# Kernel tuning notes

Hardware: AMD Instinct MI355X
Metric: run time of the kernel (lower is better)

Reference implementation:

```python
import jax, jax.numpy as jnp
import numpy as np
from jax import lax

TAU = 1.0
SIGMAS = (1.0, 1.0, 1.0)
SIGMA_CUTOFF = 2.0
SCALE_FACTORS = (0.5, 1.0)
ITERATIONS = (4, 4)
EPS = 1e-6


def _grid(shape):
    # identity sampling grid in voxel coordinates, (3, D, H, W)
    return jnp.stack(jnp.meshgrid(*[jnp.arange(s, dtype=jnp.float32) for s in shape], indexing='ij'), axis=0)


def warp(vol, flow):
    # vol (B,C,D,H,W), flow (B,3,D,H,W) voxel-space displacements; trilinear, zeros padding
    g = _grid(vol.shape[2:])
    def one_b(v, f):
        coords = g + f  # (3,D,H,W)
        def one_c(ch):
            return jax.scipy.ndimage.map_coordinates(ch, [coords[0], coords[1], coords[2]], order=1, mode='constant', cval=0.0)
        return jax.vmap(one_c)(v)
    return jax.vmap(one_b)(vol, flow)


def gaussian_smooth(x, sigmas=SIGMAS):
    # separable depthwise Gaussian, kernel radius = ceil(sigma_cutoff * sigma)
    C = x.shape[1]
    for axis, sigma in enumerate(sigmas):
        r = int(np.ceil(SIGMA_CUTOFF * sigma))
        t = jnp.arange(-r, r + 1, dtype=x.dtype)
        k = jnp.exp(-0.5 * (t / sigma) ** 2)
        k = k / k.sum()
        kshape = [1, 1, 1, 1, 1]
        kshape[2 + axis] = k.size
        w = jnp.broadcast_to(k.reshape(kshape), (C, 1) + tuple(kshape[2:]))
        x = lax.conv_general_dilated(x, w, (1, 1, 1), 'SAME', feature_group_count=C,
                                     dimension_numbers=('NCDHW', 'OIDHW', 'NCDHW'))
    return x


def _gradient(x, axis):
    # np.gradient style: central diff interior, one-sided at edges, unit spacing
    lo = lax.slice_in_dim(x, 1, 2, axis=axis) - lax.slice_in_dim(x, 0, 1, axis=axis)
    mid = (lax.slice_in_dim(x, 2, None, axis=axis) - lax.slice_in_dim(x, 0, -2, axis=axis)) * 0.5
    hi = lax.slice_in_dim(x, -1, None, axis=axis) - lax.slice_in_dim(x, -2, -1, axis=axis)
    return jnp.concatenate([lo, mid, hi], axis=axis)


def demon_forces(moving, fixed):
    # active demons: gradient of (warped) moving image, (B,1,D,H,W) -> (B,3,D,H,W)
    m = moving[:, 0]
    grads = jnp.stack([_gradient(m, 1), _gradient(m, 2), _gradient(m, 3)], axis=1)
    diff = moving - fixed  # (B,1,D,H,W)
    denom = jnp.sum(grads ** 2, axis=1, keepdims=True) + diff ** 2
    return grads * diff / (denom + EPS)


def resize_tri(x, shape):
    return jax.image.resize(x, x.shape[:2] + tuple(shape), method='trilinear')


def match_vf(vf, shape):
    if tuple(vf.shape[2:]) == tuple(shape):
        return vf
    old = vf.shape[2:]
    out = resize_tri(vf, shape)
    scale = jnp.array([s1 / s2 for s1, s2 in zip(shape, old)], dtype=vf.dtype).reshape(1, 3, 1, 1, 1)
    return out * scale


def run_level(vf, img_s, mask_s, cond_s, iters):
    def body(i, carry):
        vf, _ = carry
        warped = warp(cond_s, vf)
        f = demon_forces(warped, img_s)
        vf = vf - TAU * (f * mask_s)
        vf = gaussian_smooth(vf)
        return (vf, warped)
    return lax.fori_loop(0, iters, body, (vf, jnp.zeros_like(cond_s)))


def conv3d(x, w, b=None):
    y = lax.conv_general_dilated(x, w, (1, 1, 1), 'SAME', dimension_numbers=('NCDHW', 'OIDHW', 'NCDHW'))
    return y if b is None else y + b[None, :, None, None, None]


def instance_norm(x, eps=1e-5):
    m = x.mean(axis=(2, 3, 4), keepdims=True)
    v = x.var(axis=(2, 3, 4), keepdims=True)
    return (x - m) * lax.rsqrt(v + eps)


def mish(x):
    return x * jnp.tanh(jax.nn.softplus(x))


def setup_inputs() -> dict:
    key = jax.random.key(0)
    ks = jax.random.split(key, 8)
    S = (1, 1, 96, 96, 96)
    image = jax.random.normal(ks[0], S, dtype=jnp.float32)
    conditional = jax.random.normal(ks[1], S, dtype=jnp.float32)
    mask = jnp.ones(S, dtype=jnp.float32)
    w1 = jax.random.normal(ks[2], (32, 5, 3, 3, 3), dtype=jnp.float32) * 0.05
    w2 = jax.random.normal(ks[3], (64, 32, 3, 3, 3), dtype=jnp.float32) * 0.05
    w3 = jax.random.normal(ks[4], (32, 64, 3, 3, 3), dtype=jnp.float32) * 0.05
    w4 = jax.random.normal(ks[5], (3, 32, 3, 3, 3), dtype=jnp.float32) * 0.05
    b4 = jnp.zeros((3,), dtype=jnp.float32)
    return {"image": image, "mask": mask, "conditional": conditional,
            "w1": w1, "w2": w2, "w3": w3, "w4": w4, "b4": b4}


def reference(image, mask, conditional, w1, w2, w3, w4, b4):
    full_shape = image.shape[2:]
    vf = None
    warped = None
    for sf, iters in zip(SCALE_FACTORS, ITERATIONS):
        shp = tuple(int(s * sf) for s in full_shape)
        img_s = resize_tri(image, shp)
        mask_s = jax.image.resize(mask, mask.shape[:2] + shp, method='nearest')
        cond_s = resize_tri(conditional, shp)
        if vf is None:
            vf = jnp.zeros((image.shape[0], 3) + shp, image.dtype)
        else:
            vf = match_vf(vf, shp)
        vf, warped = run_level(vf, img_s, mask_s, cond_s, iters)
    # correction network on full-resolution level outputs
    masked_image = image * mask
    stacked = jnp.concatenate([vf, masked_image, warped], axis=1)  # (B,5,D,H,W)
    h = mish(instance_norm(conv3d(stacked, w1)))
    h = mish(instance_norm(conv3d(h, w2)))
    h = mish(instance_norm(conv3d(h, w3)))
    corr = conv3d(h, w4, b4)
    cvf = gaussian_smooth(vf + corr)
    vf_full = match_vf(vf, full_shape)
    cvf_full = match_vf(cvf, full_shape)
    corrected_warped = warp(conditional, cvf_full)
    warped_full = warp(conditional, vf_full)
    return (corrected_warped, warped_full, cvf_full, vf_full)
```

## Files before the change

kernel.cpp:

```cpp
#include <hip/hip_runtime.h>
#include <math.h>

typedef unsigned short ushort_t;
typedef __attribute__((ext_vector_type(8))) short bf16x8;
typedef __attribute__((ext_vector_type(4))) float f32x4;

constexpr int V96 = 96 * 96 * 96;
constexpr int V48 = 48 * 48 * 48;
constexpr int V98 = 98 * 98 * 98;

__device__ __constant__ float GK[5] = {
    0.05448868454964294f, 0.24420134240717082f, 0.40261994608637245f,
    0.24420134240717082f, 0.05448868454964294f };

__device__ __forceinline__ float bf2f(ushort_t u) {
    return __uint_as_float(((unsigned)u) << 16);
}
__device__ __forceinline__ ushort_t f2bf(float f) {
    unsigned x = __float_as_uint(f);
    x += 0x7fffu + ((x >> 16) & 1u);
    return (ushort_t)(x >> 16);
}
__device__ __forceinline__ bool is_bf16(const unsigned* mrw) {
    return mrw[0] == 0x3F803F80u;
}
__device__ __forceinline__ float ld_in(const void* p, int i, bool bf) {
    return bf ? bf2f(((const ushort_t*)p)[i]) : ((const float*)p)[i];
}

constexpr size_t OFF_IMG32 = 0;
constexpr size_t OFF_MSK32 = OFF_IMG32 + V96;
constexpr size_t OFF_COND32 = OFF_MSK32 + V96;
constexpr size_t OFF_VF96 = OFF_COND32 + V96;
constexpr size_t OFF_WTS = OFF_VF96 + 3 * (size_t)V96;
constexpr size_t OFF_ST = OFF_WTS + 117760;
constexpr size_t OFF_PK1 = OFF_ST + 256;
constexpr size_t OFF_PK2 = OFF_PK1 + 3584;
constexpr size_t OFF_PK3 = OFF_PK2 + 27648;
constexpr size_t OFF_PK4 = OFF_PK3 + 27648;
constexpr size_t OFF_B = OFF_PK4 + 6912;
constexpr size_t BSZF = 32 * (size_t)V98 / 2;
constexpr size_t OFF_C = OFF_B + BSZF;
constexpr size_t CSZF = 64 * (size_t)V98;
constexpr size_t WS_FLOATS = OFF_C + CSZF / 2;

constexpr size_t WOB = 117504;

template<int S>
__device__ __forceinline__ void decomp(int r, int& z, int& y, int& x) {
    z = r / (S * S); int r2 = r - z * S * S; y = r2 / S; x = r2 - y * S;
}

__global__ void cvt_in_k(const void* __restrict__ in, float* __restrict__ out, int n,
                         const unsigned* __restrict__ mrw) {
    int i = blockIdx.x * 256 + threadIdx.x;
    if (i >= n) return;
    out[i] = ld_in(in, i, is_bf16(mrw));
}
__global__ void cvt3_k(const void* __restrict__ a, const void* __restrict__ b,
                       const void* __restrict__ c, float* __restrict__ oa,
                       float* __restrict__ ob, float* __restrict__ oc,
                       const unsigned* __restrict__ mrw) {
    int i = blockIdx.x * 256 + threadIdx.x;
    if (i >= V96) return;
    bool bf = is_bf16(mrw);
    oa[i] = ld_in(a, i, bf);
    ob[i] = ld_in(b, i, bf);
    oc[i] = ld_in(c, i, bf);
}
__global__ void store_out_k(const float* __restrict__ in, void* __restrict__ out,
                            size_t off, int n, const unsigned* __restrict__ mrw) {
    int i = blockIdx.x * 256 + threadIdx.x;
    if (i >= n) return;
    if (is_bf16(mrw)) ((ushort_t*)out)[off + i] = f2bf(in[i]);
    else              ((float*)out)[off + i] = in[i];
}

template<int C>
__global__ void zero_pad_k(ushort_t* __restrict__ buf) {
    int v = blockIdx.x * 256 + threadIdx.x;
    if (v >= V98) return;
    int z = v / (98 * 98); int r = v - z * 98 * 98; int y = r / 98; int x = r - y * 98;
    if (z != 0 && z != 97 && y != 0 && y != 97 && x != 0 && x != 97) return;
    bf16x8 zv = {};
    bf16x8* p = (bf16x8*)(buf + (size_t)v * C);
#pragma unroll
    for (int c = 0; c < C / 8; ++c) p[c] = zv;
}

__global__ void pack1_k(const void* __restrict__ w, ushort_t* __restrict__ pk,
                        const unsigned* __restrict__ mrw) {
    int i = blockIdx.x * 256 + threadIdx.x;
    if (i >= 7168) return;
    bool bf = is_bf16(mrw);
    int j = i & 7, n = (i >> 3) & 15, ng = (i >> 7) & 1, tq = i >> 8;
    int co = ng * 16 + n;
    float v = (tq < 27 && j < 5) ? ld_in(w, (co * 5 + j) * 27 + tq, bf) : 0.f;
    pk[i] = f2bf(v);
}
__global__ void pack2_k(const void* __restrict__ w, ushort_t* __restrict__ pk,
                        const unsigned* __restrict__ mrw) {
    int i = blockIdx.x * 256 + threadIdx.x;
    if (i >= 55296) return;
    bool bf = is_bf16(mrw);
    int j = i & 7, n = (i >> 3) & 15, q = (i >> 7) & 3, ng = (i >> 9) & 3, t = i >> 11;
    int co = ng * 16 + n, ci = q * 8 + j;
    pk[i] = f2bf(ld_in(w, (co * 32 + ci) * 27 + t, bf));
}
__global__ void pack3_k(const void* __restrict__ w, ushort_t* __restrict__ pk,
                        const unsigned* __restrict__ mrw) {
    int i = blockIdx.x * 256 + threadIdx.x;
    if (i >= 55296) return;
    bool bf = is_bf16(mrw);
    int j = i & 7, n = (i >> 3) & 15, q = (i >> 7) & 3, ng = (i >> 9) & 1, kb = (i >> 10) & 1, t = i >> 11;
    int co = ng * 16 + n, ci = kb * 32 + q * 8 + j;
    pk[i] = f2bf(ld_in(w, (co * 64 + ci) * 27 + t, bf));
}
__global__ void pack4_k(const void* __restrict__ w, ushort_t* __restrict__ pk,
                        const unsigned* __restrict__ mrw) {
    int i = blockIdx.x * 256 + threadIdx.x;
    if (i >= 13824) return;
    bool bf = is_bf16(mrw);
    int j = i & 7, m = (i >> 3) & 15, q = (i >> 7) & 3, t = i >> 9;
    int ci = q * 8 + j;
    float v = (m < 3) ? ld_in(w, (m * 32 + ci) * 27 + t, bf) : 0.f;
    pk[i] = f2bf(v);
}

__device__ __forceinline__ int ds_wt(int i, float w[4]) {
    int j0 = 2 * i - 1;
    w[0] = 0.25f; w[1] = 0.75f; w[2] = 0.75f; w[3] = 0.25f;
    float s = 0.f;
#pragma unroll
    for (int t = 0; t < 4; ++t) { int j = j0 + t; if (j < 0 || j > 95) w[t] = 0.f; s += w[t]; }
    float inv = 1.f / s;
#pragma unroll
    for (int t = 0; t < 4; ++t) w[t] *= inv;
    return j0;
}

__global__ void down_tri_k(const float* __restrict__ in, float* __restrict__ out) {
    int idx = blockIdx.x * 256 + threadIdx.x;
    if (idx >= V48) return;
    int z, y, x; decomp<48>(idx, z, y, x);
    float wz[4], wy[4], wx[4];
    int z0 = ds_wt(z, wz), y0 = ds_wt(y, wy), x0 = ds_wt(x, wx);
    float acc = 0.f;
#pragma unroll
    for (int a = 0; a < 4; ++a) {
        int zz = z0 + a; zz = zz < 0 ? 0 : (zz > 95 ? 95 : zz);
#pragma unroll
        for (int b = 0; b < 4; ++b) {
            int yy = y0 + b; yy = yy < 0 ? 0 : (yy > 95 ? 95 : yy);
            float wzy = wz[a] * wy[b];
#pragma unroll
            for (int c = 0; c < 4; ++c) {
                int xx = x0 + c; xx = xx < 0 ? 0 : (xx > 95 ? 95 : xx);
                acc = fmaf(wzy * wx[c], in[(zz * 96 + yy) * 96 + xx], acc);
            }
        }
    }
    out[idx] = acc;
}

__global__ void down_near_k(const float* __restrict__ in, float* __restrict__ out) {
    int idx = blockIdx.x * 256 + threadIdx.x;
    if (idx >= V48) return;
    int z, y, x; decomp<48>(idx, z, y, x);
    out[idx] = in[((2 * z + 1) * 96 + (2 * y + 1)) * 96 + (2 * x + 1)];
}

__device__ __forceinline__ void up_c(int i, int& i0, float& t) {
    float s = 0.5f * (float)i - 0.25f;
    s = fminf(fmaxf(s, 0.f), 47.f);
    int ii = (int)s; if (ii > 46) ii = 46;
    i0 = ii; t = s - (float)ii;
}

__global__ void up_vf_k(const float* __restrict__ in, float* __restrict__ out) {
    int idx = blockIdx.x * 256 + threadIdx.x;
    if (idx >= 3 * V96) return;
    int c = idx / V96; int r = idx - c * V96;
    int z, y, x; decomp<96>(r, z, y, x);
    int z0, y0, x0; float tz, ty, tx;
    up_c(z, z0, tz); up_c(y, y0, ty); up_c(x, x0, tx);
    const float* p = in + (size_t)c * V48;
    float acc = 0.f;
#pragma unroll
    for (int a = 0; a < 2; ++a)
#pragma unroll
        for (int b = 0; b < 2; ++b)
#pragma unroll
            for (int d = 0; d < 2; ++d) {
                float w = (a ? tz : 1.f - tz) * (b ? ty : 1.f - ty) * (d ? tx : 1.f - tx);
                acc = fmaf(w, p[((z0 + a) * 48 + (y0 + b)) * 48 + (x0 + d)], acc);
            }
    out[idx] = 2.f * acc;
}

template<int S>
__global__ void warp_k(const float* __restrict__ vol, const float* __restrict__ flow,
                       float* __restrict__ out) {
    constexpr int S3 = S * S * S;
    int idx = blockIdx.x * 256 + threadIdx.x;
    if (idx >= S3) return;
    int z, y, x; decomp<S>(idx, z, y, x);
    float cz = (float)z + flow[idx];
    float cy = (float)y + flow[S3 + idx];
    float cx = (float)x + flow[2 * S3 + idx];
    float fz = floorf(cz), fy = floorf(cy), fx = floorf(cx);
    int iz = (int)fz, iy = (int)fy, ix = (int)fx;
    float tz = cz - fz, ty = cy - fy, tx = cx - fx;
    float acc = 0.f;
#pragma unroll
    for (int a = 0; a < 2; ++a)
#pragma unroll
        for (int b = 0; b < 2; ++b)
#pragma unroll
            for (int c = 0; c < 2; ++c) {
                int zz = iz + a, yy = iy + b, xx = ix + c;
                float w = (a ? tz : 1.f - tz) * (b ? ty : 1.f - ty) * (c ? tx : 1.f - tx);
                bool ok = ((unsigned)zz < (unsigned)S) && ((unsigned)yy < (unsigned)S) &&
                          ((unsigned)xx < (unsigned)S);
                float v = ok ? vol[(zz * S + yy) * S + xx] : 0.f;
                acc = fmaf(w, v, acc);
            }
    out[idx] = acc;
}

__global__ void warp_out_k(const float* __restrict__ vol, const float* __restrict__ flow,
                           void* __restrict__ out, size_t off,
                           const unsigned* __restrict__ mrw) {
    constexpr int S = 96, S3 = V96;
    int idx = blockIdx.x * 256 + threadIdx.x;
    if (idx >= S3) return;
    int z, y, x; decomp<S>(idx, z, y, x);
    float cz = (float)z + flow[idx];
    float cy = (float)y + flow[S3 + idx];
    float cx = (float)x + flow[2 * S3 + idx];
    float fz = floorf(cz), fy = floorf(cy), fx = floorf(cx);
    int iz = (int)fz, iy = (int)fy, ix = (int)fx;
    float tz = cz - fz, ty = cy - fy, tx = cx - fx;
    float acc = 0.f;
#pragma unroll
    for (int a = 0; a < 2; ++a)
#pragma unroll
        for (int b = 0; b < 2; ++b)
#pragma unroll
            for (int c = 0; c < 2; ++c) {
                int zz = iz + a, yy = iy + b, xx = ix + c;
                float w = (a ? tz : 1.f - tz) * (b ? ty : 1.f - ty) * (c ? tx : 1.f - tx);
                bool ok = ((unsigned)zz < (unsigned)S) && ((unsigned)yy < (unsigned)S) &&
                          ((unsigned)xx < (unsigned)S);
                float v = ok ? vol[(zz * S + yy) * S + xx] : 0.f;
                acc = fmaf(w, v, acc);
            }
    if (is_bf16(mrw)) ((ushort_t*)out)[off + idx] = f2bf(acc);
    else              ((float*)out)[off + idx] = acc;
}

template<int S>
__global__ void demon4_k(const float* __restrict__ wv, const float* __restrict__ fx_,
                         const float* __restrict__ msk, const float* __restrict__ vin,
                         float* __restrict__ vout) {
    constexpr int S3 = S * S * S;
    int u = blockIdx.x * 256 + threadIdx.x;
    if (u >= S3 / 4) return;
    int idx = u * 4;
    int z, y, x0; decomp<S>(idx, z, y, x0);
    float w[12];
    *(float4*)(w + 4) = *(const float4*)(wv + idx);
    if (x0 > 0) *(float4*)(w + 0) = *(const float4*)(wv + idx - 4);
    else { w[0] = w[1] = w[2] = w[3] = 0.f; }
    if (x0 < S - 4) *(float4*)(w + 8) = *(const float4*)(wv + idx + 4);
    else { w[8] = w[9] = w[10] = w[11] = 0.f; }
    float zp[4], zm[4], yp[4], ym[4];
    float sz = (z == 0 || z == S - 1) ? 1.f : 0.5f;
    float sy = (y == 0 || y == S - 1) ? 1.f : 0.5f;
    if (z > 0) *(float4*)zm = *(const float4*)(wv + idx - S * S);
    else { zm[0] = w[4]; zm[1] = w[5]; zm[2] = w[6]; zm[3] = w[7]; }
    if (z < S - 1) *(float4*)zp = *(const float4*)(wv + idx + S * S);
    else { zp[0] = w[4]; zp[1] = w[5]; zp[2] = w[6]; zp[3] = w[7]; }
    if (y > 0) *(float4*)ym = *(const float4*)(wv + idx - S);
    else { ym[0] = w[4]; ym[1] = w[5]; ym[2] = w[6]; ym[3] = w[7]; }
    if (y < S - 1) *(float4*)yp = *(const float4*)(wv + idx + S);
    else { yp[0] = w[4]; yp[1] = w[5]; yp[2] = w[6]; yp[3] = w[7]; }
    float fx4[4], mk4[4], v0[4], v1[4], v2[4], o0[4], o1[4], o2[4];
    *(float4*)fx4 = *(const float4*)(fx_ + idx);
    *(float4*)mk4 = *(const float4*)(msk + idx);
    *(float4*)v0 = *(const float4*)(vin + idx);
    *(float4*)v1 = *(const float4*)(vin + S3 + idx);
    *(float4*)v2 = *(const float4*)(vin + 2 * S3 + idx);
#pragma unroll
    for (int j = 0; j < 4; ++j) {
        int x = x0 + j;
        float m = w[4 + j];
        float gz = sz * (zp[j] - zm[j]);
        float gy = sy * (yp[j] - ym[j]);
        float gx = (x == 0) ? (w[j + 5] - w[j + 4])
                 : (x == S - 1) ? (w[j + 4] - w[j + 3])
                 : 0.5f * (w[j + 5] - w[j + 3]);
        float diff = m - fx4[j];
        float denom = gz * gz + gy * gy + gx * gx + diff * diff + 1e-6f;
        float r = diff / denom;
        float mk = mk4[j] * r;
        o0[j] = v0[j] - gz * mk;
        o1[j] = v1[j] - gy * mk;
        o2[j] = v2[j] - gx * mk;
    }
    *(float4*)(vout + idx) = *(float4*)o0;
    *(float4*)(vout + S3 + idx) = *(float4*)o1;
    *(float4*)(vout + 2 * S3 + idx) = *(float4*)o2;
}

template<int S, int ZC>
__global__ void smooth3d_k(const float* __restrict__ in, float* __restrict__ out) {
    constexpr int NZ = S / ZC;
    int idx = blockIdx.x * 256 + threadIdx.x;
    if (idx >= 3 * NZ * S * S) return;
    int x = idx % S;
    int y = (idx / S) % S;
    int zci = (idx / (S * S)) % NZ;
    int c = idx / (S * S * NZ);
    int z0 = zci * ZC;
    const float* p = in + (size_t)c * (S * S * S);
    float* o = out + (size_t)c * (S * S * S) + ((size_t)z0 * S + y) * S + x;
    float wx[5], wy[5];
    int xc[5], yc[5];
#pragma unroll
    for (int t = 0; t < 5; ++t) {
        int xx = x + t - 2, yy = y + t - 2;
        wx[t] = ((unsigned)xx < (unsigned)S) ? GK[t] : 0.f;
        xc[t] = xx < 0 ? 0 : (xx >= S ? S - 1 : xx);
        wy[t] = ((unsigned)yy < (unsigned)S) ? GK[t] : 0.f;
        yc[t] = yy < 0 ? 0 : (yy >= S ? S - 1 : yy);
    }
    float win[5] = {0.f, 0.f, 0.f, 0.f, 0.f};
#pragma unroll 1
    for (int k = 0; k < ZC + 4; ++k) {
        int zz = z0 - 2 + k;
        int zcl = zz < 0 ? 0 : (zz >= S ? S - 1 : zz);
        const float* ps = p + (size_t)zcl * S * S;
        float s = 0.f;
#pragma unroll
        for (int ty = 0; ty < 5; ++ty) {
            const float* pr = ps + yc[ty] * S;
            float rs = 0.f;
#pragma unroll
            for (int tx = 0; tx < 5; ++tx)
                rs = fmaf(wx[tx], pr[xc[tx]], rs);
            s = fmaf(wy[ty], rs, s);
        }
        s = ((unsigned)zz < (unsigned)S) ? s : 0.f;
        win[0] = win[1]; win[1] = win[2]; win[2] = win[3]; win[3] = win[4]; win[4] = s;
        if (k >= 4)
            o[(size_t)(k - 4) * S * S] =
                fmaf(GK[0], win[0], fmaf(GK[1], win[1], fmaf(GK[2], win[2],
                fmaf(GK[3], win[3], GK[4] * win[4]))));
    }
}

__global__ void build_st8_k(const float* __restrict__ vf, const float* __restrict__ img,
                            const float* __restrict__ msk, const float* __restrict__ wrp,
                            ushort_t* __restrict__ st8) {
    int idx = blockIdx.x * 256 + threadIdx.x;
    if (idx >= V96) return;
    int z, y, x; decomp<96>(idx, z, y, x);
    size_t pa = ((size_t)(z + 1) * 98 + (y + 1)) * 98 + (x + 1);
    union { bf16x8 v; ushort_t u[8]; } w;
    w.u[0] = f2bf(vf[idx]);
    w.u[1] = f2bf(vf[V96 + idx]);
    w.u[2] = f2bf(vf[2 * V96 + idx]);
    w.u[3] = f2bf(img[idx] * msk[idx]);
    w.u[4] = f2bf(wrp[idx]);
    w.u[5] = 0; w.u[6] = 0; w.u[7] = 0;
    *(bf16x8*)(st8 + pa * 8) = w.v;
}

__global__ __launch_bounds__(256) void conv1_mfma_k(const ushort_t* __restrict__ st8,
                                                    const ushort_t* __restrict__ pk,
                                                    ushort_t* __restrict__ out,
                                                    float* __restrict__ part) {
    const int tid = threadIdx.x;
    const int lane = tid & 63;
    const int wv = tid >> 6;
    const int ng = wv & 1;
    const int vs = wv >> 1;
    const int m = lane & 15;
    const int q = lane >> 4;
    const int x0 = blockIdx.x * 32 + vs * 16;
    const int y = blockIdx.y, z = blockIdx.z;
    f32x4 acc = {0.f, 0.f, 0.f, 0.f};
#pragma unroll
    for (int g = 0; g < 7; ++g) {
        int t = g * 4 + q;
        size_t pa = 0;
        if (t < 27) {
            int dz = t / 9, dy = (t / 3) % 3, dx = t % 3;
            pa = (((size_t)(z + dz) * 98) + (y + dy)) * 98 + (x0 + dx + m);
        }
        bf16x8 a = *(const bf16x8*)(st8 + pa * 8);
        bf16x8 b = *(const bf16x8*)(pk + (((size_t)t * 2 + ng) * 16 + m) * 8);
        acc = __builtin_amdgcn_mfma_f32_16x16x32_bf16(a, b, acc, 0, 0, 0);
    }
    const size_t pb = (((size_t)(z + 1) * 98) + (y + 1)) * 98 + (x0 + 1);
#pragma unroll
    for (int r = 0; r < 4; ++r) {
        int mm = q * 4 + r;
        out[(pb + mm) * 32 + ng * 16 + m] = f2bf(acc[r]);
    }
    float s = acc[0] + acc[1] + acc[2] + acc[3];
    float sq = acc[0] * acc[0] + acc[1] * acc[1] + acc[2] * acc[2] + acc[3] * acc[3];
    s += __shfl_xor(s, 16);  s += __shfl_xor(s, 32);
    sq += __shfl_xor(sq, 16); sq += __shfl_xor(sq, 32);
    __shared__ float red[4][2][16];
    if (q == 0) { red[wv][0][m] = s; red[wv][1][m] = sq; }
    __syncthreads();
    if (tid < 64) {
        int which = tid >> 5;
        int c = tid & 31;
        int cg = c >> 4, cm = c & 15;
        float v = red[cg][which][cm] + red[cg + 2][which][cm];
        size_t row = ((size_t)blockIdx.z * 96 + blockIdx.y) * 3 + blockIdx.x;
        part[row * 64 + tid] = v;
    }
}

__global__ __launch_bounds__(256, 3) void conv2_lds_k(const ushort_t* __restrict__ in,
                                                      const ushort_t* __restrict__ pk,
                                                      ushort_t* __restrict__ out,
                                                      float* __restrict__ part) {
    __shared__ bf16x8 sm[2160];
    const int tid = threadIdx.x;
    const int X0 = blockIdx.x * 16, Y0 = blockIdx.y * 4, Z0 = blockIdx.z * 2;
    for (int cid = tid; cid < 1728; cid += 256) {
        int r = cid / 72, c = cid - r * 72;
        int zz = r / 6, yy = r - zz * 6;
        int v = c >> 2, sub = c & 3;
        const bf16x8* gp = (const bf16x8*)(in +
            (((size_t)(Z0 + zz) * 98 + (Y0 + yy)) * 98 + X0 + v) * 32) + sub;
        sm[r * 90 + v * 5 + sub] = *gp;
    }
    __syncthreads();
    const int lane = tid & 63;
    const int wv = tid >> 6;
    const int w2 = wv >> 1;
    const int nh = wv & 1;
    const int m = lane & 15;
    const int q = lane >> 4;
    f32x4 acc[2][2][2] = {};
#pragma unroll 1
    for (int dx = 0; dx < 3; ++dx) {
        bf16x8 a[16];
#pragma unroll
        for (int zp = 0; zp < 4; ++zp)
#pragma unroll
            for (int iy = 0; iy < 4; ++iy)
                a[zp * 4 + iy] = sm[(zp * 6 + w2 * 2 + iy) * 90 + (dx + m) * 5 + q];
#pragma unroll
        for (int dz = 0; dz < 3; ++dz)
#pragma unroll
            for (int dy = 0; dy < 3; ++dy) {
                const int t = (dz * 3 + dy) * 3 + dx;
#pragma unroll
                for (int ngl = 0; ngl < 2; ++ngl) {
                    const int ng = nh * 2 + ngl;
                    bf16x8 b = *(const bf16x8*)(pk + ((((size_t)t * 4 + ng) * 4 + q) * 16 + m) * 8);
#pragma unroll
                    for (int z = 0; z < 2; ++z)
#pragma unroll
                        for (int yy = 0; yy < 2; ++yy)
                            acc[z][yy][ngl] = __builtin_amdgcn_mfma_f32_16x16x32_bf16(
                                a[(z + dz) * 4 + (yy + dy)], b, acc[z][yy][ngl], 0, 0, 0);
                }
            }
    }
#pragma unroll
    for (int z = 0; z < 2; ++z)
#pragma unroll
        for (int yy = 0; yy < 2; ++yy) {
            const size_t pb = (((size_t)(Z0 + z + 1) * 98) + (Y0 + w2 * 2 + yy + 1)) * 98 + (X0 + 1);
#pragma unroll
            for (int ngl = 0; ngl < 2; ++ngl) {
                const int ng = nh * 2 + ngl;
#pragma unroll
                for (int r = 0; r < 4; ++r) {
                    int mm = q * 4 + r;
                    out[(pb + mm) * 64 + ng * 16 + m] = f2bf(acc[z][yy][ngl][r]);
                }
            }
        }
    float s0 = 0.f, q0 = 0.f, s1 = 0.f, q1 = 0.f;
#pragma unroll
    for (int z = 0; z < 2; ++z)
#pragma unroll
        for (int yy = 0; yy < 2; ++yy)
#pragma unroll
            for (int r = 0; r < 4; ++r) {
                float v0 = acc[z][yy][0][r]; s0 += v0; q0 = fmaf(v0, v0, q0);
                float v1 = acc[z][yy][1][r]; s1 += v1; q1 = fmaf(v1, v1, q1);
            }
    s0 += __shfl_xor(s0, 16); s0 += __shfl_xor(s0, 32);
    q0 += __shfl_xor(q0, 16); q0 += __shfl_xor(q0, 32);
    s1 += __shfl_xor(s1, 16); s1 += __shfl_xor(s1, 32);
    q1 += __shfl_xor(q1, 16); q1 += __shfl_xor(q1, 32);
    __shared__ float red[4][2][2][16];
    if (q == 0) {
        red[wv][0][0][m] = s0; red[wv][0][1][m] = q0;
        red[wv][1][0][m] = s1; red[wv][1][1][m] = q1;
    }
    __syncthreads();
    if (tid < 128) {
        int which = tid >> 6;
        int c = tid & 63;
        int cnh = (c >> 5) & 1, cngl = (c >> 4) & 1, cm = c & 15;
        float v = red[cnh][cngl][which][cm] + red[2 + cnh][cngl][which][cm];
        size_t row = ((size_t)blockIdx.z * 24 + blockIdx.y) * 6 + blockIdx.x;
        part[row * 128 + tid] = v;
    }
}

__global__ __launch_bounds__(256, 4) void conv3_lds_k(const ushort_t* __restrict__ in,
                                                      const ushort_t* __restrict__ pk,
                                                      ushort_t* __restrict__ out,
                                                      float* __restrict__ part) {
    __shared__ bf16x8 sm[2160];
    const int tid = threadIdx.x;
    const int X0 = blockIdx.x * 16, Y0 = blockIdx.y * 4, Z0 = blockIdx.z * 2;
    const int lane = tid & 63;
    const int wv = tid >> 6;
    const int w2 = wv >> 1;
    const int ng = wv & 1;
    const int m = lane & 15;
    const int q = lane >> 4;
    f32x4 acc[2][2] = {};
#pragma unroll 1
    for (int kb = 0; kb < 2; ++kb) {
        if (kb) __syncthreads();
        for (int cid = tid; cid < 1728; cid += 256) {
            int r = cid / 72, c = cid - r * 72;
            int zz = r / 6, yy = r - zz * 6;
            int v = c >> 2, sub = c & 3;
            const bf16x8* gp = (const bf16x8*)(in +
                (((size_t)(Z0 + zz) * 98 + (Y0 + yy)) * 98 + X0 + v) * 64 + kb * 32) + sub;
            sm[r * 90 + v * 5 + sub] = *gp;
        }
        __syncthreads();
#pragma unroll 1
        for (int dx = 0; dx < 3; ++dx) {
            bf16x8 a[16];
#pragma unroll
            for (int zp = 0; zp < 4; ++zp)
#pragma unroll
                for (int iy = 0; iy < 4; ++iy)
                    a[zp * 4 + iy] = sm[(zp * 6 + w2 * 2 + iy) * 90 + (dx + m) * 5 + q];
#pragma unroll
            for (int dz = 0; dz < 3; ++dz)
#pragma unroll
                for (int dy = 0; dy < 3; ++dy) {
                    const int t = (dz * 3 + dy) * 3 + dx;
                    bf16x8 b = *(const bf16x8*)(pk +
                        (((((size_t)t * 2 + kb) * 2 + ng) * 4 + q) * 16 + m) * 8);
#pragma unroll
                    for (int z = 0; z < 2; ++z)
#pragma unroll
                        for (int yy = 0; yy < 2; ++yy)
                            acc[z][yy] = __builtin_amdgcn_mfma_f32_16x16x32_bf16(
                                a[(z + dz) * 4 + (yy + dy)], b, acc[z][yy], 0, 0, 0);
                }
        }
    }
#pragma unroll
    for (int z = 0; z < 2; ++z)
#pragma unroll
        for (int yy = 0; yy < 2; ++yy) {
            const size_t pb = (((size_t)(Z0 + z + 1) * 98) + (Y0 + w2 * 2 + yy + 1)) * 98 + (X0 + 1);
#pragma unroll
            for (int r = 0; r < 4; ++r) {
                int mm = q * 4 + r;
                out[(pb + mm) * 32 + ng * 16 + m] = f2bf(acc[z][yy][r]);
            }
        }
    float s = 0.f, sq = 0.f;
#pragma unroll
    for (int z = 0; z < 2; ++z)
#pragma unroll
        for (int yy = 0; yy < 2; ++yy)
#pragma unroll
            for (int r = 0; r < 4; ++r) {
                float v = acc[z][yy][r]; s += v; sq = fmaf(v, v, sq);
            }
    s += __shfl_xor(s, 16);  s += __shfl_xor(s, 32);
    sq += __shfl_xor(sq, 16); sq += __shfl_xor(sq, 32);
    __shared__ float red[4][2][16];
    if (q == 0) { red[wv][0][m] = s; red[wv][1][m] = sq; }
    __syncthreads();
    if (tid < 64) {
        int which = tid >> 5;
        int c = tid & 31;
        int cg = c >> 4, cm = c & 15;
        float v = red[cg][which][cm] + red[cg + 2][which][cm];
        size_t row = ((size_t)blockIdx.z * 24 + blockIdx.y) * 6 + blockIdx.x;
        part[row * 64 + tid] = v;
    }
}

__global__ __launch_bounds__(384) void conv4_mfma_k(const ushort_t* __restrict__ in,
                                                    const ushort_t* __restrict__ pk,
                                                    const float* __restrict__ bias,
                                                    const float* __restrict__ vf,
                                                    float* __restrict__ out) {
    const int lane = threadIdx.x & 63;
    const int wv = threadIdx.x >> 6;
    const int n = lane & 15;
    const int q = lane >> 4;
    const int x0 = wv * 16;
    const int y = blockIdx.y, z = blockIdx.z;
    f32x4 acc = {0.f, 0.f, 0.f, 0.f};
#pragma unroll 1
    for (int dz = 0; dz < 3; ++dz)
#pragma unroll
        for (int dy = 0; dy < 3; ++dy)
#pragma unroll
            for (int dx = 0; dx < 3; ++dx) {
                const int t = (dz * 3 + dy) * 3 + dx;
                bf16x8 a = *(const bf16x8*)(pk + (((size_t)t * 4 + q) * 16 + n) * 8);
                bf16x8 b = *(const bf16x8*)(in +
                    ((((size_t)(z + dz) * 98) + (y + dy)) * 98 + (x0 + dx + n)) * 32 + q * 8);
                acc = __builtin_amdgcn_mfma_f32_16x16x32_bf16(a, b, acc, 0, 0, 0);
            }
    if (q == 0) {
        int ob = ((z * 96) + y) * 96 + x0 + n;
#pragma unroll
        for (int r = 0; r < 3; ++r)
            out[(size_t)r * V96 + ob] = acc[r] + bias[r] + vf[(size_t)r * V96 + ob];
    }
}

template<int C>
__global__ void finalize2_k(const float* __restrict__ part, int nrows,
                            float* __restrict__ st) {
    const int c = blockIdx.x;
    const int tid = threadIdx.x;
    float s = 0.f, q = 0.f;
    for (int r = tid; r < nrows; r += 256) {
        s += part[(size_t)r * 2 * C + c];
        q += part[(size_t)r * 2 * C + C + c];
    }
    __shared__ float ls[256], lq[256];
    ls[tid] = s; lq[tid] = q; __syncthreads();
    for (int off = 128; off; off >>= 1) {
        if (tid < off) { ls[tid] += ls[tid + off]; lq[tid] += lq[tid + off]; }
        __syncthreads();
    }
    if (tid == 0) {
        float mean = ls[0] * (1.f / 884736.f);
        float var = lq[0] * (1.f / 884736.f) - mean * mean;
        st[2 * c] = mean;
        st[2 * c + 1] = rsqrtf(var + 1e-5f);
    }
}

template<int C>
__global__ void inmish8_k(ushort_t* __restrict__ buf, const float* __restrict__ st) {
    size_t u = (size_t)blockIdx.x * 256 + threadIdx.x;
    if (u >= (size_t)C * V96 / 8) return;
    size_t i0 = u * 8;
    int v = (int)(i0 / C);
    int c0 = (int)(i0 % C);
    int z, y, x; decomp<96>(v, z, y, x);
    size_t pa = (((size_t)(z + 1) * 98 + (y + 1)) * 98 + (x + 1)) * C + c0;
    union { bf16x8 vv; ushort_t us[8]; } ld, stv;
    ld.vv = *(const bf16x8*)(buf + pa);
#pragma unroll
    for (int j = 0; j < 8; ++j) {
        int c = c0 + j;
        float mean = st[2 * c];
        float rstd = st[2 * c + 1];
        float val = (bf2f(ld.us[j]) - mean) * rstd;
        float vc = fminf(val, 30.f);
        float e = __builtin_amdgcn_exp2f(vc * 1.44269504088896f);
        float n = e * (e + 2.f);
        float r = n * __builtin_amdgcn_rcpf(n + 2.f);
        stv.us[j] = f2bf(val * r);
    }
    *(bf16x8*)(buf + pa) = stv.vv;
}

extern "C" void kernel_launch(void* const* d_in, const int* in_sizes, int n_in,
                              void* d_out, int out_size, void* d_ws, size_t ws_size,
                              hipStream_t stream) {
    const void* image_raw = d_in[0];
    const unsigned* mask_raw = (const unsigned*)d_in[1];
    const void* cond_raw = d_in[2];
    float* ws = (float*)d_ws;

    if (ws_size < WS_FLOATS * sizeof(float)) return;

    float* img32 = ws + OFF_IMG32;
    float* msk32 = ws + OFF_MSK32;
    float* cond32 = ws + OFF_COND32;
    float* vf96 = ws + OFF_VF96;
    float* wts = ws + OFF_WTS;
    float* st = ws + OFF_ST;
    ushort_t* pk1 = (ushort_t*)(ws + OFF_PK1);
    ushort_t* pk2 = (ushort_t*)(ws + OFF_PK2);
    ushort_t* pk3 = (ushort_t*)(ws + OFF_PK3);
    ushort_t* pk4 = (ushort_t*)(ws + OFF_PK4);
    float* Bf = ws + OFF_B;
    float* Cf = ws + OFF_C;

    float* t96a = Bf;
    float* l48 = Bf + 6 * (size_t)V96;
    float* img48 = l48;
    float* cond48 = l48 + V48;
    float* mask48 = l48 + 2 * (size_t)V48;
    float* warp48 = l48 + 3 * (size_t)V48;
    float* vf48   = l48 + 4 * (size_t)V48;
    float* t48a   = l48 + 7 * (size_t)V48;

    float* warped96 = Cf;
    ushort_t* st8 = (ushort_t*)(Cf + V96);
    float* cvtmp    = Cf + 3 * (size_t)V96;

    ushort_t* h1 = (ushort_t*)Bf;
    ushort_t* h2 = (ushort_t*)Cf;

    float* part = img32;

    auto g1 = [](int n) { return dim3((unsigned)((n + 255) / 256)); };

    cvt3_k<<<g1(V96), 256, 0, stream>>>(image_raw, (const void*)mask_raw, cond_raw,
                                        img32, msk32, cond32, mask_raw);
    cvt_in_k<<<1, 256, 0, stream>>>(d_in[7], wts + WOB, 3, mask_raw);
    pack1_k<<<g1(7168), 256, 0, stream>>>(d_in[3], pk1, mask_raw);
    pack2_k<<<g1(55296), 256, 0, stream>>>(d_in[4], pk2, mask_raw);
    pack3_k<<<g1(55296), 256, 0, stream>>>(d_in[5], pk3, mask_raw);
    pack4_k<<<g1(13824), 256, 0, stream>>>(d_in[6], pk4, mask_raw);

    down_tri_k<<<g1(V48), 256, 0, stream>>>(img32, img48);
    down_tri_k<<<g1(V48), 256, 0, stream>>>(cond32, cond48);
    down_near_k<<<g1(V48), 256, 0, stream>>>(msk32, mask48);
    hipMemsetAsync(vf48, 0, 3 * (size_t)V48 * sizeof(float), stream);

    for (int it = 0; it < 4; ++it) {
        warp_k<48><<<g1(V48), 256, 0, stream>>>(cond48, vf48, warp48);
        demon4_k<48><<<g1(V48 / 4), 256, 0, stream>>>(warp48, img48, mask48, vf48, t48a);
        smooth3d_k<48, 6><<<g1(3 * 8 * 48 * 48), 256, 0, stream>>>(t48a, vf48);
    }

    up_vf_k<<<g1(3 * V96), 256, 0, stream>>>(vf48, vf96);

    for (int it = 0; it < 4; ++it) {
        warp_k<96><<<g1(V96), 256, 0, stream>>>(cond32, vf96, warped96);
        demon4_k<96><<<g1(V96 / 4), 256, 0, stream>>>(warped96, img32, msk32, vf96, t96a);
        smooth3d_k<96, 12><<<g1(3 * 8 * 96 * 96), 256, 0, stream>>>(t96a, vf96);
    }

    zero_pad_k<32><<<g1(V98), 256, 0, stream>>>((ushort_t*)Bf);
    zero_pad_k<8><<<g1(V98), 256, 0, stream>>>(st8);
    build_st8_k<<<g1(V96), 256, 0, stream>>>(vf96, img32, msk32, warped96, st8);

    conv1_mfma_k<<<dim3(3, 96, 96), 256, 0, stream>>>(st8, pk1, h1, part);
    finalize2_k<32><<<32, 256, 0, stream>>>(part, 27648, st + 0);
    inmish8_k<32><<<g1(32 * V96 / 8), 256, 0, stream>>>(h1, st + 0);

    zero_pad_k<64><<<g1(V98), 256, 0, stream>>>((ushort_t*)Cf);

    conv2_lds_k<<<dim3(6, 24, 48), 256, 0, stream>>>(h1, pk2, h2, part);
    finalize2_k<64><<<64, 256, 0, stream>>>(part, 6912, st + 64);
    inmish8_k<64><<<g1(64 * V96 / 8), 256, 0, stream>>>(h2, st + 64);

    conv3_lds_k<<<dim3(6, 24, 48), 256, 0, stream>>>(h2, pk3, h1, part);
    finalize2_k<32><<<32, 256, 0, stream>>>(part, 6912, st + 192);
    inmish8_k<32><<<g1(32 * V96 / 8), 256, 0, stream>>>(h1, st + 192);

    conv4_mfma_k<<<dim3(1, 96, 96), 384, 0, stream>>>(h1, pk4, wts + WOB, vf96, cvtmp);

    smooth3d_k<96, 12><<<g1(3 * 8 * 96 * 96), 256, 0, stream>>>(cvtmp, Cf);

    store_out_k<<<g1(3 * V96), 256, 0, stream>>>(Cf, d_out, 2 * (size_t)V96, 3 * V96, mask_raw);
    warp_out_k<<<g1(V96), 256, 0, stream>>>(cond32, Cf, d_out, 0, mask_raw);
    warp_out_k<<<g1(V96), 256, 0, stream>>>(cond32, vf96, d_out, (size_t)V96, mask_raw);
    store_out_k<<<g1(3 * V96), 256, 0, stream>>>(vf96, d_out, 5 * (size_t)V96, 3 * V96, mask_raw);
}
```

Baseline: 1.241 ms.

## Fuse instance-norm+mish into conv2/conv3 tile loads and cache conv4 weights in LDS

The first two instance-norm+mish passes now run inside the LDS staging loops of conv2 and conv3, which zero halo voxels explicitly, so two inmish kernels and a zero-pad launch are dropped. This saves two full read-modify-write passes over the 32- and 64-channel activation buffers. The cost is that each voxel is normalised several times because tiles overlap, and the load loops do more ALU work. Separately, conv4 stages its packed weights in shared memory and preloads all 27 input fragments before issuing MFMAs, which raises register pressure.

```diff
diff --git a/kernel.cpp b/kernel.cpp
--- a/kernel.cpp
+++ b/kernel.cpp
@@ -26,6 +26,13 @@
 }
 __device__ __forceinline__ float ld_in(const void* p, int i, bool bf) {
     return bf ? bf2f(((const ushort_t*)p)[i]) : ((const float*)p)[i];
+}
+__device__ __forceinline__ float mishf(float val) {
+    float vc = fminf(val, 30.f);
+    float e = __builtin_amdgcn_exp2f(vc * 1.44269504088896f);
+    float n = e * (e + 2.f);
+    float r = n * __builtin_amdgcn_rcpf(n + 2.f);
+    return val * r;
 }
 
 constexpr size_t OFF_IMG32 = 0;
@@ -429,17 +436,35 @@
 __global__ __launch_bounds__(256, 3) void conv2_lds_k(const ushort_t* __restrict__ in,
                                                       const ushort_t* __restrict__ pk,
                                                       ushort_t* __restrict__ out,
-                                                      float* __restrict__ part) {
+                                                      float* __restrict__ part,
+                                                      const float* __restrict__ st) {
     __shared__ bf16x8 sm[2160];
     const int tid = threadIdx.x;
     const int X0 = blockIdx.x * 16, Y0 = blockIdx.y * 4, Z0 = blockIdx.z * 2;
+    const int sub0 = tid & 3;
+    float mean8[8], rstd8[8];
+#pragma unroll
+    for (int j = 0; j < 8; ++j) {
+        mean8[j] = st[2 * (sub0 * 8 + j)];
+        rstd8[j] = st[2 * (sub0 * 8 + j) + 1];
+    }
     for (int cid = tid; cid < 1728; cid += 256) {
         int r = cid / 72, c = cid - r * 72;
         int zz = r / 6, yy = r - zz * 6;
         int v = c >> 2, sub = c & 3;
-        const bf16x8* gp = (const bf16x8*)(in +
-            (((size_t)(Z0 + zz) * 98 + (Y0 + yy)) * 98 + X0 + v) * 32) + sub;
-        sm[r * 90 + v * 5 + sub] = *gp;
+        int pz = Z0 + zz, py = Y0 + yy, px = X0 + v;
+        union { bf16x8 vv; ushort_t u[8]; } w;
+        w.vv = *((const bf16x8*)(in + (((size_t)pz * 98 + py) * 98 + px) * 32) + sub);
+        bool halo = (pz == 0) | (pz == 97) | (py == 0) | (py == 97) | (px == 0) | (px == 97);
+        if (halo) {
+            bf16x8 zv = {};
+            w.vv = zv;
+        } else {
+#pragma unroll
+            for (int j = 0; j < 8; ++j)
+                w.u[j] = f2bf(mishf((bf2f(w.u[j]) - mean8[j]) * rstd8[j]));
+        }
+        sm[r * 90 + v * 5 + sub] = w.vv;
     }
     __syncthreads();
     const int lane = tid & 63;
@@ -523,7 +548,8 @@
 __global__ __launch_bounds__(256, 4) void conv3_lds_k(const ushort_t* __restrict__ in,
                                                       const ushort_t* __restrict__ pk,
                                                       ushort_t* __restrict__ out,
-                                                      float* __restrict__ part) {
+                                                      float* __restrict__ part,
+                                                      const float* __restrict__ st) {
     __shared__ bf16x8 sm[2160];
     const int tid = threadIdx.x;
     const int X0 = blockIdx.x * 16, Y0 = blockIdx.y * 4, Z0 = blockIdx.z * 2;
@@ -533,17 +559,35 @@
     const int ng = wv & 1;
     const int m = lane & 15;
     const int q = lane >> 4;
+    const int sub0 = tid & 3;
     f32x4 acc[2][2] = {};
 #pragma unroll 1
     for (int kb = 0; kb < 2; ++kb) {
+        float mean8[8], rstd8[8];
+#pragma unroll
+        for (int j = 0; j < 8; ++j) {
+            int c = kb * 32 + sub0 * 8 + j;
+            mean8[j] = st[2 * c];
+            rstd8[j] = st[2 * c + 1];
+        }
         if (kb) __syncthreads();
         for (int cid = tid; cid < 1728; cid += 256) {
             int r = cid / 72, c = cid - r * 72;
             int zz = r / 6, yy = r - zz * 6;
             int v = c >> 2, sub = c & 3;
-            const bf16x8* gp = (const bf16x8*)(in +
-                (((size_t)(Z0 + zz) * 98 + (Y0 + yy)) * 98 + X0 + v) * 64 + kb * 32) + sub;
-            sm[r * 90 + v * 5 + sub] = *gp;
+            int pz = Z0 + zz, py = Y0 + yy, px = X0 + v;
+            union { bf16x8 vv; ushort_t u[8]; } w;
+            w.vv = *((const bf16x8*)(in + (((size_t)pz * 98 + py) * 98 + px) * 64 + kb * 32) + sub);
+            bool halo = (pz == 0) | (pz == 97) | (py == 0) | (py == 97) | (px == 0) | (px == 97);
+            if (halo) {
+                bf16x8 zv = {};
+                w.vv = zv;
+            } else {
+#pragma unroll
+                for (int j = 0; j < 8; ++j)
+                    w.u[j] = f2bf(mishf((bf2f(w.u[j]) - mean8[j]) * rstd8[j]));
+            }
+            sm[r * 90 + v * 5 + sub] = w.vv;
         }
         __syncthreads();
 #pragma unroll 1
@@ -610,25 +654,30 @@
                                                     const float* __restrict__ bias,
                                                     const float* __restrict__ vf,
                                                     float* __restrict__ out) {
-    const int lane = threadIdx.x & 63;
-    const int wv = threadIdx.x >> 6;
+    __shared__ ushort_t smpk[13824];
+    const int tid = threadIdx.x;
+    for (int i = tid; i < 1728; i += 384)
+        ((bf16x8*)smpk)[i] = ((const bf16x8*)pk)[i];
+    __syncthreads();
+    const int lane = tid & 63;
+    const int wv = tid >> 6;
     const int n = lane & 15;
     const int q = lane >> 4;
     const int x0 = wv * 16;
     const int y = blockIdx.y, z = blockIdx.z;
+    bf16x8 bv[27];
+#pragma unroll
+    for (int t = 0; t < 27; ++t) {
+        const int dz = t / 9, dy = (t / 3) % 3, dx = t % 3;
+        bv[t] = *(const bf16x8*)(in +
+            ((((size_t)(z + dz) * 98) + (y + dy)) * 98 + (x0 + dx + n)) * 32 + q * 8);
+    }
     f32x4 acc = {0.f, 0.f, 0.f, 0.f};
-#pragma unroll 1
-    for (int dz = 0; dz < 3; ++dz)
-#pragma unroll
-        for (int dy = 0; dy < 3; ++dy)
-#pragma unroll
-            for (int dx = 0; dx < 3; ++dx) {
-                const int t = (dz * 3 + dy) * 3 + dx;
-                bf16x8 a = *(const bf16x8*)(pk + (((size_t)t * 4 + q) * 16 + n) * 8);
-                bf16x8 b = *(const bf16x8*)(in +
-                    ((((size_t)(z + dz) * 98) + (y + dy)) * 98 + (x0 + dx + n)) * 32 + q * 8);
-                acc = __builtin_amdgcn_mfma_f32_16x16x32_bf16(a, b, acc, 0, 0, 0);
-            }
+#pragma unroll
+    for (int t = 0; t < 27; ++t) {
+        bf16x8 a = *(const bf16x8*)(smpk + ((t * 4 + q) * 16 + n) * 8);
+        acc = __builtin_amdgcn_mfma_f32_16x16x32_bf16(a, bv[t], acc, 0, 0, 0);
+    }
     if (q == 0) {
         int ob = ((z * 96) + y) * 96 + x0 + n;
 #pragma unroll
@@ -675,14 +724,8 @@
 #pragma unroll
     for (int j = 0; j < 8; ++j) {
         int c = c0 + j;
-        float mean = st[2 * c];
-        float rstd = st[2 * c + 1];
-        float val = (bf2f(ld.us[j]) - mean) * rstd;
-        float vc = fminf(val, 30.f);
-        float e = __builtin_amdgcn_exp2f(vc * 1.44269504088896f);
-        float n = e * (e + 2.f);
-        float r = n * __builtin_amdgcn_rcpf(n + 2.f);
-        stv.us[j] = f2bf(val * r);
+        float val = (bf2f(ld.us[j]) - st[2 * c]) * st[2 * c + 1];
+        stv.us[j] = f2bf(mishf(val));
     }
     *(bf16x8*)(buf + pa) = stv.vv;
 }
@@ -763,15 +806,11 @@
 
     conv1_mfma_k<<<dim3(3, 96, 96), 256, 0, stream>>>(st8, pk1, h1, part);
     finalize2_k<32><<<32, 256, 0, stream>>>(part, 27648, st + 0);
-    inmish8_k<32><<<g1(32 * V96 / 8), 256, 0, stream>>>(h1, st + 0);
-
-    zero_pad_k<64><<<g1(V98), 256, 0, stream>>>((ushort_t*)Cf);
-
-    conv2_lds_k<<<dim3(6, 24, 48), 256, 0, stream>>>(h1, pk2, h2, part);
+
+    conv2_lds_k<<<dim3(6, 24, 48), 256, 0, stream>>>(h1, pk2, h2, part, st + 0);
     finalize2_k<64><<<64, 256, 0, stream>>>(part, 6912, st + 64);
-    inmish8_k<64><<<g1(64 * V96 / 8), 256, 0, stream>>>(h2, st + 64);
-
-    conv3_lds_k<<<dim3(6, 24, 48), 256, 0, stream>>>(h2, pk3, h1, part);
+
+    conv3_lds_k<<<dim3(6, 24, 48), 256, 0, stream>>>(h2, pk3, h1, part, st + 64);
     finalize2_k<32><<<32, 256, 0, stream>>>(part, 6912, st + 192);
     inmish8_k<32><<<g1(32 * V96 / 8), 256, 0, stream>>>(h1, st + 192);
 
```

Measured after the change: 1.208 ms. -2.6%, faster.
